# Optimization experiments

Measured on AMD Instinct MI355X. Metric: run time of the kernel, lower is better.

Reference implementation:

```python
import jax, jax.numpy as jnp
import numpy as np

T, D_ENC, H, D_EMB, VOCAB = 4000, 1024, 1024, 512, 8192
V = VOCAB + 1  # + blank
P = 800
TEMPERATURE = 1.0


def setup_inputs() -> dict:
    key = jax.random.key(0)
    ks = jax.random.split(key, 8)
    s = lambda d: 1.0 / np.sqrt(d)
    return {
        'enc_out': jax.random.normal(ks[0], (T, D_ENC), jnp.float32),
        'embedding': jax.random.normal(ks[1], (V, D_EMB), jnp.float32) * s(D_EMB),
        'W_ih': jax.random.normal(ks[2], (4 * H, D_EMB), jnp.float32) * s(D_EMB),
        'W_hh': jax.random.normal(ks[3], (4 * H, H), jnp.float32) * s(H),
        'b_lstm': jnp.zeros((4 * H,), jnp.float32),
        'W_pred': jax.random.normal(ks[4], (D_ENC, H), jnp.float32) * s(H),
        'b_pred': jnp.zeros((D_ENC,), jnp.float32),
        'W_join': jax.random.normal(ks[5], (V, D_ENC), jnp.float32) * s(D_ENC),
        'b_join': jnp.zeros((V,), jnp.float32),
        'phonemes': jax.random.randint(ks[6], (P,), 0, VOCAB, jnp.int32),
    }


def reference(enc_out, embedding, W_ih, W_hh, b_lstm, W_pred, b_pred, W_join, b_join, phonemes):
    blank_idx = embedding.shape[0] - 1
    n_phon = phonemes.shape[0]

    def predict_step(tok, h, c):
        # one-token RNNT predictor: embed -> LSTM cell -> projection to joiner dim
        x = embedding[tok]
        gates = x @ W_ih.T + h @ W_hh.T + b_lstm  # [4H]
        i, f, g, o = jnp.split(gates, 4)
        i, f, o = jax.nn.sigmoid(i), jax.nn.sigmoid(f), jax.nn.sigmoid(o)
        c2 = f * c + i * jnp.tanh(g)
        h2 = o * jnp.tanh(c2)
        pred = h2 @ W_pred.T + b_pred  # [D_ENC]
        return pred, h2, c2

    def step(carry, enc_t):
        tok, h, c, tp = carry
        pred, h2, c2 = predict_step(tok, h, c)
        logits = (jax.nn.relu(enc_t + pred) @ W_join.T + b_join) / TEMPERATURE
        logp = jax.nn.log_softmax(logits)  # [V]
        pick = jnp.argmax(logp)
        phon_done = tp >= n_phon
        is_blank = (pick == blank_idx) | phon_done
        next_phon = phonemes[jnp.minimum(tp, n_phon - 1)]
        prediction = jnp.where(is_blank, blank_idx, next_phon)
        # blank: keep hypothesis token/state; non-blank: advance to phoneme + new state
        tok2 = jnp.where(is_blank, tok, next_phon)
        h3 = jnp.where(is_blank, h, h2)
        c3 = jnp.where(is_blank, c, c2)
        tp2 = tp + jnp.where(is_blank, 0, 1)
        return (tok2, h3, c3, tp2), (logp, prediction, ~phon_done)

    # initial predictor pass with blank token from zero state (mirrors the warm-up predict call)
    h0 = jnp.zeros((W_hh.shape[1],), enc_out.dtype)
    c0 = jnp.zeros_like(h0)
    _, h_init, c_init = predict_step(jnp.int32(blank_idx), h0, c0)
    carry0 = (jnp.int32(blank_idx), h_init, c_init, jnp.int32(0))
    _, (alignment, predictions, valid) = jax.lax.scan(step, carry0, enc_out)
    return alignment, predictions, valid
```

## Files before the change

kernel.cpp:

```cpp
#include <hip/hip_runtime.h>
#include <math.h>

#define TT     4000
#define DENC   1024
#define HD     1024
#define DEMB   512
#define VD     8193
#define NPH    800
#define BLANK  8192
#define NWG    256
#define NTHR   512
#define CHUNK_M 800
#define NSTEP  (NPH + 2)
#define NSTEPP 802
#define NVT    65
#define NP     129
#define CHUNK  256

typedef __bf16 bf16x4 __attribute__((ext_vector_type(4)));
typedef __bf16 bf16x8 __attribute__((ext_vector_type(8)));
typedef float  f32x16 __attribute__((ext_vector_type(16)));

#define MEMSET_BYTES 20480
#define WSF_HX     1024
#define WSF_HHIST  5120
#define WSF_PREDS  826368
#define WSF_GXT    826368
#define WSF_PMAX   1646592
#define WSF_PSUM   2162592
#define WSF_PARG   2678592
#define WSF_LSE    3194592
#define WSF_AMAX   3198592
#define WSF_XBF    3199616
#define WSF_W16    4903552
#define WSF_END    9163392
#define NEED_MFMA  ((size_t)WSF_END * 4)
#define TST_IDX    512
#define F_PMAX 1646592
#define F_PSUM 1906592
#define F_PARG 2166592
#define F_LSE  2426592

#define GEMM_SMEM  12800
#define CHAIN_SMEM ((16 * NSTEPP + 2048 + 64) * 4)
#define JOIN_SMEM  (65536 + 128)
#define S_XH   0
#define S_GS   3072
#define S_C4   3088
#define S_TOK  3264
#define S_RED  4066
#define S_AMAX 4082
#define SMEM_FLOATS_F32 4352
#define SMEM_BYTES_F32 (SMEM_FLOATS_F32 * 4)


__device__ __forceinline__ float dot4(float4 a, float4 b, float acc) {
  acc = fmaf(a.x, b.x, acc); acc = fmaf(a.y, b.y, acc);
  acc = fmaf(a.z, b.z, acc); acc = fmaf(a.w, b.w, acc);
  return acc;
}
__device__ __forceinline__ float sigmf(float x) { return 1.f / (1.f + expf(-x)); }
__device__ __forceinline__ float sigm_fast(float x) { return 1.f / (1.f + __expf(-x)); }
__device__ __forceinline__ float tanh_fast(float x) {
  float e = __expf(2.f * x);
  return 1.f - 2.f / (e + 1.f);
}

__device__ __forceinline__ void combine3(float& m, float& s, int& am,
                                         float om, float os, int oa) {
  float mm = fmaxf(m, om);
  s = s * __expf(m - mm) + os * __expf(om - mm);
  if (om > m || (om == m && oa < am)) am = oa;
  m = mm;
}

__device__ __forceinline__ void gload16(const void* g, void* l) {
  __builtin_amdgcn_global_load_lds(
      (const __attribute__((address_space(1))) unsigned int*)g,
      (__attribute__((address_space(3))) unsigned int*)l, 16, 0, 0);
}

__device__ __forceinline__ float ld_coh(const float* p) {
  return __hip_atomic_load((const float*)p, __ATOMIC_RELAXED, __HIP_MEMORY_SCOPE_AGENT);
}

__device__ __forceinline__ void light_barrier(unsigned* flags, unsigned& ep) {
  unsigned* arrive  = flags;
  unsigned* release = flags + 256;
  __builtin_amdgcn_s_waitcnt(0);
  __syncthreads();
  if (blockIdx.x == 0) {
    int tid = threadIdx.x;
    if (tid > 0 && tid < NWG) {
      while (__hip_atomic_load(&arrive[tid], __ATOMIC_RELAXED, __HIP_MEMORY_SCOPE_AGENT) != ep) {}
    }
    __syncthreads();
    if (tid == 0)
      __hip_atomic_store(release, ep, __ATOMIC_RELAXED, __HIP_MEMORY_SCOPE_AGENT);
  } else {
    if (threadIdx.x == 0) {
      __hip_atomic_store(&arrive[blockIdx.x], ep, __ATOMIC_RELAXED, __HIP_MEMORY_SCOPE_AGENT);
      while (__hip_atomic_load(release, __ATOMIC_RELAXED, __HIP_MEMORY_SCOPE_AGENT) != ep) {}
    }
    __syncthreads();
  }
  asm volatile("" ::: "memory");
  ep++;
}

__device__ __forceinline__ void heavy_barrier(unsigned* flags) {
  unsigned* bar = flags + 257;
  __syncthreads();
  if (threadIdx.x == 0) {
    __threadfence();
    unsigned g = __hip_atomic_load(&bar[1], __ATOMIC_RELAXED, __HIP_MEMORY_SCOPE_AGENT);
    unsigned v = __hip_atomic_fetch_add(&bar[0], 1u, __ATOMIC_RELAXED, __HIP_MEMORY_SCOPE_AGENT);
    if (v == (unsigned)(NWG - 1)) {
      __hip_atomic_store(&bar[0], 0u, __ATOMIC_RELAXED, __HIP_MEMORY_SCOPE_AGENT);
      __hip_atomic_store(&bar[1], g + 1u, __ATOMIC_RELEASE, __HIP_MEMORY_SCOPE_AGENT);
    } else {
      while (__hip_atomic_load(&bar[1], __ATOMIC_RELAXED, __HIP_MEMORY_SCOPE_AGENT) == g)
        __builtin_amdgcn_s_sleep(1);
    }
    __threadfence();
  }
  __syncthreads();
}

__device__ void xbf_fill(const float* enc, const float* preds, __bf16* dst,
                         int t0, int K, int pi0, int g0, int gs) {
  int total = K << 8;
  for (int q = g0; q < total; q += gs) {
    int j = q >> 8, seg = q & 255;
    int pi = (pi0 < 0) ? NPH : pi0 + j;
    float4 e = ((const float4*)(enc + (size_t)(t0 + j) * 1024))[seg];
    float4 p = ((const float4*)(preds + (size_t)pi * 1024))[seg];
    bf16x4 r;
    r[0] = (__bf16)fmaxf(e.x + p.x, 0.f);
    r[1] = (__bf16)fmaxf(e.y + p.y, 0.f);
    r[2] = (__bf16)fmaxf(e.z + p.z, 0.f);
    r[3] = (__bf16)fmaxf(e.w + p.w, 0.f);
    *(bf16x4*)(dst + (size_t)j * 1024 + (seg << 2)) = r;
  }
}

__device__ void joiner_tiles(const __bf16* W16, const __bf16* xrows, const float* bj,
                             float* out_align, float* pmax, float* psum, int* parg,
                             char* smc, int t0, int K, int tile0, int tstride) {
  const int tid = threadIdx.x;
  const int wid = tid >> 6, lane = tid & 63;
  const int wj = wid & 3, wv = wid >> 2;
  const int l31 = lane & 31, lhi = lane >> 5;
  const int jt_n = (K + 127) >> 7;
  const int ntiles = jt_n * NVT;

  for (int tile = tile0; tile < ntiles; tile += tstride) {
    const int vt = tile % NVT, jt = tile / NVT;
    const int v0 = vt << 7, j0 = jt << 7;
    f32x16 acc0, acc1;
    #pragma unroll
    for (int i = 0; i < 16; ++i) { acc0[i] = 0.f; acc1[i] = 0.f; }

    auto stage = [&](int db, int kb) {
      char* wb = smc + db * 32768;
      char* xb = wb + 16384;
      #pragma unroll
      for (int p = 0; p < 2; ++p) {
        int sbase = p * 512 + wid * 64;
        int s = sbase + lane;
        int ks = s >> 7, r = s & 127;
        gload16(W16 + (size_t)(v0 + r) * 1024 + kb + ks * 8, wb + sbase * 16);
        gload16(xrows + (size_t)(j0 + r) * 1024 + kb + ks * 8, xb + sbase * 16);
      }
    };

    stage(0, 0);
    __syncthreads();
    int db = 0;
    for (int kb16 = 0; kb16 < 16; ++kb16) {
      if (kb16 < 15) stage(db ^ 1, (kb16 + 1) << 6);
      const char* wb = smc + db * 32768;
      const char* xb = wb + 16384;
      #pragma unroll
      for (int k16 = 0; k16 < 4; ++k16) {
        int ks = k16 * 2 + lhi;
        bf16x8 a  = *(const bf16x8*)(xb + ((ks << 7) + (wj << 5) + l31) * 16);
        bf16x8 b0 = *(const bf16x8*)(wb + ((ks << 7) + (wv << 6) + l31) * 16);
        bf16x8 b1 = *(const bf16x8*)(wb + ((ks << 7) + (wv << 6) + 32 + l31) * 16);
        acc0 = __builtin_amdgcn_mfma_f32_32x32x16_bf16(a, b0, acc0, 0, 0, 0);
        acc1 = __builtin_amdgcn_mfma_f32_32x32x16_bf16(a, b1, acc1, 0, 0, 0);
      }
      __syncthreads();
      db ^= 1;
    }

    const int v_0 = v0 + (wv << 6) + l31;
    const int v_1 = v_0 + 32;
    const float bj0 = (v_0 < VD) ? bj[v_0] : 0.f;
    const float bj1 = (v_1 < VD) ? bj[v_1] : 0.f;
    const int jbase = j0 + (wj << 5) + 4 * lhi;
    const bool npok = (v0 + (wv << 6)) < VD;
    const int np = (v0 >> 6) + wv;
    #pragma unroll
    for (int reg = 0; reg < 16; ++reg) {
      int j = jbase + (reg & 3) + 8 * (reg >> 2);
      bool jok = j < K;
      float lg0 = acc0[reg] + bj0;
      float lg1 = acc1[reg] + bj1;
      if (jok) {
        size_t ro = (size_t)(t0 + j) * VD;
        if (v_0 < VD) out_align[ro + v_0] = lg0;
        if (v_1 < VD) out_align[ro + v_1] = lg1;
      }
      float l0 = (v_0 < VD) ? lg0 : -1e30f;
      float l1 = (v_1 < VD) ? lg1 : -1e30f;
      float m = fmaxf(l0, l1);
      float ss = 0.f;
      if (v_0 < VD) ss += __expf(l0 - m);
      if (v_1 < VD) ss += __expf(l1 - m);
      int am = (l1 > l0) ? v_1 : v_0;
      #pragma unroll
      for (int msk = 1; msk <= 16; msk <<= 1) {
        float om = __shfl_xor(m, msk, 64);
        float os = __shfl_xor(ss, msk, 64);
        int oa = __shfl_xor(am, msk, 64);
        float mm = fmaxf(m, om);
        ss = ss * __expf(m - mm) + os * __expf(om - mm);
        if (om > m || (om == m && oa < am)) am = oa;
        m = mm;
      }
      if (l31 == 0 && jok && npok) {
        size_t pb = (size_t)(t0 + j) * NP + np;
        __hip_atomic_store(&pmax[pb], m, __ATOMIC_RELAXED, __HIP_MEMORY_SCOPE_AGENT);
        __hip_atomic_store(&psum[pb], ss, __ATOMIC_RELAXED, __HIP_MEMORY_SCOPE_AGENT);
        __hip_atomic_store(&parg[pb], am, __ATOMIC_RELAXED, __HIP_MEMORY_SCOPE_AGENT);
      }
    }
  }
}

__device__ __forceinline__ void merge_row129(const float* pmax, const float* psum,
                                             const int* parg, int row, int lane,
                                             float& m, float& s, int& am) {
  size_t b = (size_t)row * NP;
  m = ld_coh(pmax + b + lane);
  s = ld_coh(psum + b + lane);
  am = __hip_atomic_load(&parg[b + lane], __ATOMIC_RELAXED, __HIP_MEMORY_SCOPE_AGENT);
  {
    int i2 = lane + 64;
    float om = ld_coh(pmax + b + i2);
    float os = ld_coh(psum + b + i2);
    int oa = __hip_atomic_load(&parg[b + i2], __ATOMIC_RELAXED, __HIP_MEMORY_SCOPE_AGENT);
    combine3(m, s, am, om, os, oa);
  }
  if (lane == 0) {
    float om = ld_coh(pmax + b + 128);
    float os = ld_coh(psum + b + 128);
    int oa = __hip_atomic_load(&parg[b + 128], __ATOMIC_RELAXED, __HIP_MEMORY_SCOPE_AGENT);
    combine3(m, s, am, om, os, oa);
  }
  #pragma unroll
  for (int msk = 32; msk; msk >>= 1) {
    float om = __shfl_xor(m, msk, 64);
    float os = __shfl_xor(s, msk, 64);
    int oa = __shfl_xor(am, msk, 64);
    combine3(m, s, am, om, os, oa);
  }
}

__global__ __launch_bounds__(512) void wconv_kernel(const float* __restrict__ Wjoin,
                                                    float* wsf) {
  __bf16* w16 = (__bf16*)(wsf + WSF_W16);
  int g0 = blockIdx.x * 512 + threadIdx.x;
  int gs = gridDim.x * 512;
  for (int q = g0; q < VD * 256; q += gs) {
    int v = q >> 8, seg = q & 255;
    float4 w4 = ((const float4*)(Wjoin + (size_t)v * 1024))[seg];
    bf16x4 r;
    r[0] = (__bf16)w4.x; r[1] = (__bf16)w4.y; r[2] = (__bf16)w4.z; r[3] = (__bf16)w4.w;
    *(bf16x4*)(w16 + (size_t)v * 1024 + (seg << 2)) = r;
  }
}

__global__ __launch_bounds__(512) void gx_kernel(
    const float* __restrict__ Wih, const float* __restrict__ emb,
    const float* __restrict__ bl, const int* __restrict__ phon, float* wsf) {
  extern __shared__ float sm[];
  float* Wt = sm;
  float* Xt = sm + 2112;
  float* gxT = wsf + WSF_GXT;
  const int tid = threadIdx.x;
  const int tx = tid & 31, ty = tid >> 5;
  int ntiles = 32 * 13;
  for (int tile = blockIdx.x; tile < ntiles; tile += gridDim.x) {
    int vt = tile & 31, jt = tile >> 5;
    int v0 = vt * 128, j0 = jt * 64;
    float acc[4][4];
    #pragma unroll
    for (int a = 0; a < 4; ++a)
      #pragma unroll
      for (int q = 0; q < 4; ++q) acc[a][q] = 0.f;
    for (int kk = 0; kk < DEMB; kk += 16) {
      {
        int r = tid >> 2, seg = tid & 3;
        float4 wv = ((const float4*)(Wih + (size_t)(v0 + r) * DEMB + kk))[seg];
        Wt[(seg * 4 + 0) * 132 + r] = wv.x;
        Wt[(seg * 4 + 1) * 132 + r] = wv.y;
        Wt[(seg * 4 + 2) * 132 + r] = wv.z;
        Wt[(seg * 4 + 3) * 132 + r] = wv.w;
      }
      if (tid < 256) {
        int r = tid >> 2, seg = tid & 3;
        int j = j0 + r;
        float4 xv = make_float4(0.f, 0.f, 0.f, 0.f);
        if (j < NSTEP) {
          int tok = (j < 2) ? BLANK : phon[j - 2];
          xv = ((const float4*)(emb + (size_t)tok * DEMB + kk))[seg];
        }
        Xt[(seg * 4 + 0) * 68 + r] = xv.x;
        Xt[(seg * 4 + 1) * 68 + r] = xv.y;
        Xt[(seg * 4 + 2) * 68 + r] = xv.z;
        Xt[(seg * 4 + 3) * 68 + r] = xv.w;
      }
      __syncthreads();
      #pragma unroll
      for (int k = 0; k < 16; ++k) {
        float4 a = *(const float4*)(Wt + k * 132 + (tx << 2));
        float4 bq = *(const float4*)(Xt + k * 68 + (ty << 2));
        acc[0][0] = fmaf(a.x, bq.x, acc[0][0]); acc[1][0] = fmaf(a.y, bq.x, acc[1][0]);
        acc[2][0] = fmaf(a.z, bq.x, acc[2][0]); acc[3][0] = fmaf(a.w, bq.x, acc[3][0]);
        acc[0][1] = fmaf(a.x, bq.y, acc[0][1]); acc[1][1] = fmaf(a.y, bq.y, acc[1][1]);
        acc[2][1] = fmaf(a.z, bq.y, acc[2][1]); acc[3][1] = fmaf(a.w, bq.y, acc[3][1]);
        acc[0][2] = fmaf(a.x, bq.z, acc[0][2]); acc[1][2] = fmaf(a.y, bq.z, acc[1][2]);
        acc[2][2] = fmaf(a.z, bq.z, acc[2][2]); acc[3][2] = fmaf(a.w, bq.z, acc[3][2]);
        acc[0][3] = fmaf(a.x, bq.w, acc[0][3]); acc[1][3] = fmaf(a.y, bq.w, acc[1][3]);
        acc[2][3] = fmaf(a.z, bq.w, acc[2][3]); acc[3][3] = fmaf(a.w, bq.w, acc[3][3]);
      }
      __syncthreads();
    }
    int vb = v0 + (tx << 2), jb0 = j0 + (ty << 2);
    #pragma unroll
    for (int jj = 0; jj < 4; ++jj) {
      int j = jb0 + jj;
      if (j >= NSTEP) continue;
      #pragma unroll
      for (int q = 0; q < 4; ++q)
        gxT[(size_t)(vb + q) * NSTEPP + j] = acc[q][jj] + bl[vb + q];
    }
  }
}

__global__ __launch_bounds__(NTHR) void chain_kernel(const float* __restrict__ Whh,
                                                     float* wsf) {
  extern __shared__ float sm[];
  float* gxl = sm;
  float* hb  = sm + 16 * NSTEPP;
  float* GS  = hb + 2048;
  const int tid = threadIdx.x;
  const int w = tid >> 6, l = tid & 63;
  const int b = blockIdx.x;
  const float* gxT = wsf + WSF_GXT;
  float* hhist = wsf + WSF_HHIST;
  unsigned long long* hx = (unsigned long long*)(wsf + WSF_HX);

  float4 W0[4], W1[4];
  {
    int rr0 = 2 * w, rr1 = 2 * w + 1;
    int gr0 = ((rr0 >> 2) << 10) + 4 * b + (rr0 & 3);
    int gr1 = ((rr1 >> 2) << 10) + 4 * b + (rr1 & 3);
    const float4* h0 = (const float4*)(Whh + (size_t)gr0 * HD);
    const float4* h1 = (const float4*)(Whh + (size_t)gr1 * HD);
    #pragma unroll
    for (int i = 0; i < 4; ++i) { W0[i] = h0[l + 64 * i]; W1[i] = h1[l + 64 * i]; }
  }
  for (int rr = 0; rr < 16; ++rr) {
    int gr = ((rr >> 2) << 10) + 4 * b + (rr & 3);
    for (int s = tid; s < NSTEP; s += NTHR)
      gxl[rr * NSTEPP + s] = gxT[(size_t)gr * NSTEPP + s];
  }
  for (int i = tid; i < 1024; i += NTHR) hb[i] = 0.f;
  __syncthreads();

  float c_reg = 0.f;
  for (int s = 0; s < NSTEP; ++s) {
    int p = s & 1;
    const float4* h4 = (const float4*)(hb + p * 1024);
    float a0 = 0.f, a1 = 0.f;
    #pragma unroll
    for (int i = 0; i < 4; ++i) {
      float4 hv = h4[l + 64 * i];
      a0 = dot4(W0[i], hv, a0);
      a1 = dot4(W1[i], hv, a1);
    }
    #pragma unroll
    for (int m = 32; m; m >>= 1) {
      a0 += __shfl_xor(a0, m, 64);
      a1 += __shfl_xor(a1, m, 64);
    }
    if (l == 0) { GS[2 * w] = a0; GS[2 * w + 1] = a1; }
    __syncthreads();
    if (tid < 4) {
      int j = tid;
      float gi = GS[j]      + gxl[j * NSTEPP + s];
      float gf = GS[4 + j]  + gxl[(4 + j) * NSTEPP + s];
      float gg = GS[8 + j]  + gxl[(8 + j) * NSTEPP + s];
      float go = GS[12 + j] + gxl[(12 + j) * NSTEPP + s];
      float c2 = sigm_fast(gf) * c_reg + sigm_fast(gi) * tanh_fast(gg);
      float h2 = sigm_fast(go) * tanh_fast(c2);
      c_reg = c2;
      int cell = 4 * b + j;
      hhist[(size_t)s * HD + cell] = h2;
      unsigned long long pk = ((unsigned long long)(unsigned)(s + 1) << 32)
                            | (unsigned long long)__float_as_uint(h2);
      __hip_atomic_store(&hx[(p ^ 1) * 1024 + cell], pk,
                         __ATOMIC_RELAXED, __HIP_MEMORY_SCOPE_AGENT);
    }
    if (s + 1 < NSTEP) {
      unsigned tg = (unsigned)(s + 1);
      const unsigned long long* src = hx + (p ^ 1) * 1024;
      unsigned long long v0, v1;
      do {
        v0 = __hip_atomic_load(&src[2 * tid],     __ATOMIC_RELAXED, __HIP_MEMORY_SCOPE_AGENT);
        v1 = __hip_atomic_load(&src[2 * tid + 1], __ATOMIC_RELAXED, __HIP_MEMORY_SCOPE_AGENT);
      } while ((unsigned)(v0 >> 32) != tg || (unsigned)(v1 >> 32) != tg);
      float* dst = hb + (p ^ 1) * 1024 + 2 * tid;
      dst[0] = __uint_as_float((unsigned)v0);
      dst[1] = __uint_as_float((unsigned)v1);
    }
    __syncthreads();
  }
}

__global__ __launch_bounds__(512) void preds_kernel(
    const float* __restrict__ Wpred, const float* __restrict__ bp, float* wsf) {
  extern __shared__ float sm[];
  float* Wt = sm;
  float* Xt = sm + 2112;
  const float* hhist = wsf + WSF_HHIST;
  float* preds = wsf + WSF_PREDS;
  const int tid = threadIdx.x;
  const int tx = tid & 31, ty = tid >> 5;
  int ntiles = 8 * 13;
  for (int tile = blockIdx.x; tile < ntiles; tile += gridDim.x) {
    int vt = tile & 7, jt = tile >> 3;
    int v0 = vt * 128, j0 = jt * 64;
    float acc[4][4];
    #pragma unroll
    for (int a = 0; a < 4; ++a)
      #pragma unroll
      for (int q = 0; q < 4; ++q) acc[a][q] = 0.f;
    for (int kk = 0; kk < 1024; kk += 16) {
      {
        int r = tid >> 2, seg = tid & 3;
        float4 wv = ((const float4*)(Wpred + (size_t)(v0 + r) * HD + kk))[seg];
        Wt[(seg * 4 + 0) * 132 + r] = wv.x;
        Wt[(seg * 4 + 1) * 132 + r] = wv.y;
        Wt[(seg * 4 + 2) * 132 + r] = wv.z;
        Wt[(seg * 4 + 3) * 132 + r] = wv.w;
      }
      if (tid < 256) {
        int r = tid >> 2, seg = tid & 3;
        int j = j0 + r;
        float4 xv = make_float4(0.f, 0.f, 0.f, 0.f);
        if (j <= NPH) xv = ((const float4*)(hhist + (size_t)(j + 1) * HD + kk))[seg];
        Xt[(seg * 4 + 0) * 68 + r] = xv.x;
        Xt[(seg * 4 + 1) * 68 + r] = xv.y;
        Xt[(seg * 4 + 2) * 68 + r] = xv.z;
        Xt[(seg * 4 + 3) * 68 + r] = xv.w;
      }
      __syncthreads();
      #pragma unroll
      for (int k = 0; k < 16; ++k) {
        float4 a = *(const float4*)(Wt + k * 132 + (tx << 2));
        float4 bq = *(const float4*)(Xt + k * 68 + (ty << 2));
        acc[0][0] = fmaf(a.x, bq.x, acc[0][0]); acc[1][0] = fmaf(a.y, bq.x, acc[1][0]);
        acc[2][0] = fmaf(a.z, bq.x, acc[2][0]); acc[3][0] = fmaf(a.w, bq.x, acc[3][0]);
        acc[0][1] = fmaf(a.x, bq.y, acc[0][1]); acc[1][1] = fmaf(a.y, bq.y, acc[1][1]);
        acc[2][1] = fmaf(a.z, bq.y, acc[2][1]); acc[3][1] = fmaf(a.w, bq.y, acc[3][1]);
        acc[0][2] = fmaf(a.x, bq.z, acc[0][2]); acc[1][2] = fmaf(a.y, bq.z, acc[1][2]);
        acc[2][2] = fmaf(a.z, bq.z, acc[2][2]); acc[3][2] = fmaf(a.w, bq.z, acc[3][2]);
        acc[0][3] = fmaf(a.x, bq.w, acc[0][3]); acc[1][3] = fmaf(a.y, bq.w, acc[1][3]);
        acc[2][3] = fmaf(a.z, bq.w, acc[2][3]); acc[3][3] = fmaf(a.w, bq.w, acc[3][3]);
      }
      __syncthreads();
    }
    int vb = v0 + (tx << 2), jb0 = j0 + (ty << 2);
    #pragma unroll
    for (int jj = 0; jj < 4; ++jj) {
      int j = jb0 + jj;
      if (j > NPH) continue;
      #pragma unroll
      for (int q = 0; q < 4; ++q)
        preds[(size_t)j * 1024 + vb + q] = acc[q][jj] + bp[vb + q];
    }
  }
}

__global__ void xspec_kernel(const float* __restrict__ enc, float* wsf) {
  xbf_fill(enc, wsf + WSF_PREDS, (__bf16*)(wsf + WSF_XBF), 0, CHUNK_M, 0,
           blockIdx.x * blockDim.x + threadIdx.x, gridDim.x * blockDim.x);
}

__global__ __launch_bounds__(NTHR) void joinspec_kernel(const float* __restrict__ bj,
                                                        float* out, float* wsf) {
  extern __shared__ float sm[];
  joiner_tiles((__bf16*)(wsf + WSF_W16), (__bf16*)(wsf + WSF_XBF), bj, out,
               wsf + WSF_PMAX, wsf + WSF_PSUM, (int*)(wsf + WSF_PARG),
               (char*)sm, 0, CHUNK_M, blockIdx.x, gridDim.x);
}

__global__ __launch_bounds__(NTHR) void decode_coop(
    const float* enc, const float* bj, const int* phon, float* out, float* wsf) {
  extern __shared__ float sm[];
  char* smc = (char*)sm;
  unsigned* flags = (unsigned*)wsf;
  float* preds = wsf + WSF_PREDS;
  float* pmax = wsf + WSF_PMAX;
  float* psum = wsf + WSF_PSUM;
  int* parg = (int*)(wsf + WSF_PARG);
  float* lse = wsf + WSF_LSE;
  int* amaxws = (int*)(wsf + WSF_AMAX);
  __bf16* xbf = (__bf16*)(wsf + WSF_XBF);
  __bf16* w16 = (__bf16*)(wsf + WSF_W16);
  float* out_pred  = out + (size_t)TT * VD;
  float* out_valid = out + (size_t)TT * VD + TT;

  const int tid = threadIdx.x;
  const int wid = tid >> 6, lane = tid & 63;
  unsigned ep = 1;
  int t = 0, tp = 0, iter = 0;

  while (t < TT && tp < NPH) {
    int K = CHUNK_M;
    if (TT - t < K) K = TT - t;
    if (NPH - tp < K) K = NPH - tp;
    if (iter > 0) {
      heavy_barrier(flags);
      xbf_fill(enc, preds, xbf, t, K, tp, blockIdx.x * NTHR + tid, gridDim.x * NTHR);
      heavy_barrier(flags);
      joiner_tiles(w16, xbf, bj, out, pmax, psum, parg, smc, t, K,
                   blockIdx.x, gridDim.x);
    }
    light_barrier(flags, ep);
    for (int j = blockIdx.x * 8 + wid; j < K; j += gridDim.x * 8) {
      float m, s; int am;
      merge_row129(pmax, psum, parg, t + j, lane, m, s, am);
      if (lane == 0) {
        __hip_atomic_store(&amaxws[j], am, __ATOMIC_RELAXED, __HIP_MEMORY_SCOPE_AGENT);
        lse[t + j] = m + logf(s);
      }
    }
    light_barrier(flags, ep);
    int cand = K;
    for (int idx = tid; idx < K; idx += NTHR) {
      int a = __hip_atomic_load(&amaxws[idx], __ATOMIC_RELAXED, __HIP_MEMORY_SCOPE_AGENT);
      if (a == BLANK && idx < cand) cand = idx;
    }
    #pragma unroll
    for (int msk = 32; msk; msk >>= 1) cand = min(cand, __shfl_xor(cand, msk, 64));
    int* red = (int*)(smc + 65536);
    if (lane == 0) red[wid] = cand;
    __syncthreads();
    if (tid == 0) {
      int mn = red[0];
      for (int w2 = 1; w2 < 8; ++w2) mn = min(mn, red[w2]);
      red[8] = mn;
    }
    __syncthreads();
    int jb = red[8];
    __syncthreads();
    int nacc = (jb < K) ? jb + 1 : K;
    int nadv = (jb < K) ? jb : K;
    if (blockIdx.x == 0) {
      for (int j = tid; j < nacc; j += NTHR) {
        out_pred[t + j] = (j == jb) ? (float)BLANK : (float)phon[tp + j];
        out_valid[t + j] = 1.f;
      }
    }
    t += nacc; tp += nadv; ++iter;
  }

  if (t < TT) {
    xbf_fill(enc, preds, xbf + (size_t)(t - 800) * 1024, t, TT - t, -1,
             blockIdx.x * NTHR + tid, gridDim.x * NTHR);
  }
  if (blockIdx.x == 0 && tid == 0) ((int*)wsf)[TST_IDX] = t;
}

__global__ __launch_bounds__(NTHR) void jointail_kernel(const float* __restrict__ bj,
                                                        float* out, float* wsf) {
  extern __shared__ float sm[];
  int t = ((const int*)wsf)[TST_IDX];
  if (t >= TT) return;
  joiner_tiles((__bf16*)(wsf + WSF_W16),
               (__bf16*)(wsf + WSF_XBF) + (size_t)(t - 800) * 1024, bj, out,
               wsf + WSF_PMAX, wsf + WSF_PSUM, (int*)(wsf + WSF_PARG),
               (char*)sm, t, TT - t, blockIdx.x, gridDim.x);
}

__global__ __launch_bounds__(NTHR) void mergetail_kernel(float* out, float* wsf) {
  int t = ((const int*)wsf)[TST_IDX];
  float* lse = wsf + WSF_LSE;
  float* out_pred  = out + (size_t)TT * VD;
  float* out_valid = out + (size_t)TT * VD + TT;
  const int wid = threadIdx.x >> 6, lane = threadIdx.x & 63;
  for (int row = t + blockIdx.x * 8 + wid; row < TT; row += gridDim.x * 8) {
    float m, s; int am;
    merge_row129(wsf + WSF_PMAX, wsf + WSF_PSUM, (const int*)(wsf + WSF_PARG),
                 row, lane, m, s, am);
    if (lane == 0) {
      lse[row] = m + logf(s);
      out_pred[row] = (float)BLANK;
      out_valid[row] = 0.f;
    }
  }
}

__global__ __launch_bounds__(256) void sub_kernel(float* out, const float* wsf) {
  const float* lse = wsf + WSF_LSE;
  for (int row = blockIdx.x; row < TT; row += gridDim.x) {
    float l = lse[row];
    float* p = out + (size_t)row * VD;
    for (int i = threadIdx.x; i < VD; i += 256) p[i] -= l;
  }
}

struct Ctx {
  const float *enc, *emb, *Wih, *Whh, *bl, *Wpred, *bp, *Wjoin, *bj;
  const int* phon;
  unsigned long long* hx;
  float *hhist, *preds, *pmax, *psum, *lse;
  int* parg;
  unsigned* flags;
  float *out_align, *out_pred, *out_valid;
};

__device__ void chain_all_legacy(const Ctx& C, float* sm) {
  const int tid = threadIdx.x;
  const int w = tid >> 6, l = tid & 63;
  const int b = blockIdx.x;
  int* tok_sm = (int*)(sm + S_TOK);
  for (int s = tid; s < NSTEP; s += NTHR)
    tok_sm[s] = (s < 2) ? BLANK : C.phon[s - 2];
  float4 W0[6], W1[6];
  {
    int rr0 = 2 * w, rr1 = 2 * w + 1;
    int gr0 = ((rr0 >> 2) << 10) + 4 * b + (rr0 & 3);
    int gr1 = ((rr1 >> 2) << 10) + 4 * b + (rr1 & 3);
    const float4* ih0 = (const float4*)(C.Wih + (size_t)gr0 * DEMB);
    const float4* hh0 = (const float4*)(C.Whh + (size_t)gr0 * HD);
    const float4* ih1 = (const float4*)(C.Wih + (size_t)gr1 * DEMB);
    const float4* hh1 = (const float4*)(C.Whh + (size_t)gr1 * HD);
    W0[0] = ih0[l];       W0[1] = ih0[64 + l];
    W0[2] = hh0[l];       W0[3] = hh0[64 + l];
    W0[4] = hh0[128 + l]; W0[5] = hh0[192 + l];
    W1[0] = ih1[l];       W1[1] = ih1[64 + l];
    W1[2] = hh1[l];       W1[3] = hh1[64 + l];
    W1[4] = hh1[128 + l]; W1[5] = hh1[192 + l];
  }
  float bi = 0.f, bf = 0.f, bg = 0.f, bo = 0.f;
  if (tid < 4) {
    bi = C.bl[4 * b + tid];
    bf = C.bl[1024 + 4 * b + tid];
    bg = C.bl[2048 + 4 * b + tid];
    bo = C.bl[3072 + 4 * b + tid];
    sm[S_C4 + tid] = 0.f;
  }
  for (int i = tid; i < 1536; i += NTHR) sm[S_XH + i] = 0.f;
  if (tid < 512) sm[S_XH + tid] = C.emb[(size_t)BLANK * DEMB + tid];
  __syncthreads();
  unsigned long long* hx = C.hx;
  for (int s = 0; s < NSTEP; ++s) {
    int p = s & 1;
    const float4* xh4 = (const float4*)(sm + S_XH + p * 1536);
    float a0 = 0.f, a1 = 0.f;
    #pragma unroll
    for (int i = 0; i < 6; ++i) {
      float4 v = xh4[i * 64 + l];
      a0 = dot4(W0[i], v, a0);
      a1 = dot4(W1[i], v, a1);
    }
    #pragma unroll
    for (int m = 32; m; m >>= 1) {
      a0 += __shfl_xor(a0, m, 64);
      a1 += __shfl_xor(a1, m, 64);
    }
    if (l == 0) { sm[S_GS + 2 * w] = a0; sm[S_GS + 2 * w + 1] = a1; }
    if (s + 1 < NSTEP && tid < 512)
      sm[S_XH + (1 - p) * 1536 + tid] = C.emb[(size_t)tok_sm[s + 1] * DEMB + tid];
    __syncthreads();
    if (tid < 4) {
      int j = tid;
      float gi = sm[S_GS + j]      + bi;
      float gf = sm[S_GS + 4 + j]  + bf;
      float gg = sm[S_GS + 8 + j]  + bg;
      float go = sm[S_GS + 12 + j] + bo;
      float cc = sm[S_C4 + j];
      float c2 = sigmf(gf) * cc + sigmf(gi) * tanhf(gg);
      float h2 = sigmf(go) * tanhf(c2);
      sm[S_C4 + j] = c2;
      int cell = 4 * b + j;
      C.hhist[(size_t)s * HD + cell] = h2;
      unsigned long long pk = ((unsigned long long)(unsigned)(s + 1) << 32)
                            | (unsigned long long)__float_as_uint(h2);
      __hip_atomic_store(&hx[(1 - p) * 1024 + cell], pk,
                         __ATOMIC_RELAXED, __HIP_MEMORY_SCOPE_AGENT);
    }
    if (s + 1 < NSTEP) {
      unsigned tg = (unsigned)(s + 1);
      #pragma unroll
      for (int kq = 0; kq < 2; ++kq) {
        int k = tid + kq * 512;
        unsigned long long v;
        do {
          v = __hip_atomic_load(&hx[(1 - p) * 1024 + k],
                                __ATOMIC_RELAXED, __HIP_MEMORY_SCOPE_AGENT);
        } while ((unsigned)(v >> 32) != tg);
        sm[S_XH + (1 - p) * 1536 + 512 + k] = __uint_as_float((unsigned)v);
      }
    }
    __syncthreads();
  }
}

__device__ void preds_gemm_legacy(const Ctx& C, float* sm) {
  float* Wt = sm;
  float* Xt = sm + 2112;
  const int tid = threadIdx.x;
  const int tx = tid & 31, ty = tid >> 5;
  int ntiles = 8 * 13;
  for (int tile = blockIdx.x; tile < ntiles; tile += NWG) {
    int vt = tile & 7, jt = tile >> 3;
    int v0 = vt * 128, j0 = jt * 64;
    float acc[4][4];
    #pragma unroll
    for (int a = 0; a < 4; ++a)
      #pragma unroll
      for (int q = 0; q < 4; ++q) acc[a][q] = 0.f;
    for (int kk = 0; kk < 1024; kk += 16) {
      {
        int r = tid >> 2, seg = tid & 3;
        float4 wv = ((const float4*)(C.Wpred + (size_t)(v0 + r) * HD + kk))[seg];
        Wt[(seg * 4 + 0) * 132 + r] = wv.x;
        Wt[(seg * 4 + 1) * 132 + r] = wv.y;
        Wt[(seg * 4 + 2) * 132 + r] = wv.z;
        Wt[(seg * 4 + 3) * 132 + r] = wv.w;
      }
      if (tid < 256) {
        int r = tid >> 2, seg = tid & 3;
        int j = j0 + r;
        float4 xv = make_float4(0.f, 0.f, 0.f, 0.f);
        if (j <= NPH) xv = ((const float4*)(C.hhist + (size_t)(j + 1) * HD + kk))[seg];
        Xt[(seg * 4 + 0) * 68 + r] = xv.x;
        Xt[(seg * 4 + 1) * 68 + r] = xv.y;
        Xt[(seg * 4 + 2) * 68 + r] = xv.z;
        Xt[(seg * 4 + 3) * 68 + r] = xv.w;
      }
      __syncthreads();
      #pragma unroll
      for (int k = 0; k < 16; ++k) {
        float4 a = *(const float4*)(Wt + k * 132 + (tx << 2));
        float4 bq = *(const float4*)(Xt + k * 68 + (ty << 2));
        acc[0][0] = fmaf(a.x, bq.x, acc[0][0]); acc[1][0] = fmaf(a.y, bq.x, acc[1][0]);
        acc[2][0] = fmaf(a.z, bq.x, acc[2][0]); acc[3][0] = fmaf(a.w, bq.x, acc[3][0]);
        acc[0][1] = fmaf(a.x, bq.y, acc[0][1]); acc[1][1] = fmaf(a.y, bq.y, acc[1][1]);
        acc[2][1] = fmaf(a.z, bq.y, acc[2][1]); acc[3][1] = fmaf(a.w, bq.y, acc[3][1]);
        acc[0][2] = fmaf(a.x, bq.z, acc[0][2]); acc[1][2] = fmaf(a.y, bq.z, acc[1][2]);
        acc[2][2] = fmaf(a.z, bq.z, acc[2][2]); acc[3][2] = fmaf(a.w, bq.z, acc[3][2]);
        acc[0][3] = fmaf(a.x, bq.w, acc[0][3]); acc[1][3] = fmaf(a.y, bq.w, acc[1][3]);
        acc[2][3] = fmaf(a.z, bq.w, acc[2][3]); acc[3][3] = fmaf(a.w, bq.w, acc[3][3]);
      }
      __syncthreads();
    }
    int vb = v0 + (tx << 2), jb0 = j0 + (ty << 2);
    #pragma unroll
    for (int jj = 0; jj < 4; ++jj) {
      int j = jb0 + jj;
      if (j > NPH) continue;
      #pragma unroll
      for (int q = 0; q < 4; ++q)
        C.preds[(size_t)j * 1024 + vb + q] = acc[q][jj] + C.bp[vb + q];
    }
  }
}

__device__ void joiner_gemm_f32(const Ctx& C, float* sm, int t0, int K, int pi0) {
  float* Wt = sm;
  float* Xt = sm + 2112;
  const int tid = threadIdx.x;
  const int tx = tid & 31, ty = tid >> 5;
  int jt_n = (K + 63) >> 6;
  int ntiles = jt_n * NVT;
  for (int tile = blockIdx.x; tile < ntiles; tile += NWG) {
    int vt = tile % NVT, jt = tile / NVT;
    int v0 = vt * 128, j0 = jt * 64;
    float acc[4][4];
    #pragma unroll
    for (int a = 0; a < 4; ++a)
      #pragma unroll
      for (int q = 0; q < 4; ++q) acc[a][q] = 0.f;
    for (int kk = 0; kk < 1024; kk += 16) {
      {
        int r = tid >> 2, seg = tid & 3;
        int v = v0 + r;
        float4 wv = make_float4(0.f, 0.f, 0.f, 0.f);
        if (v < VD) wv = ((const float4*)(C.Wjoin + (size_t)v * 1024 + kk))[seg];
        Wt[(seg * 4 + 0) * 132 + r] = wv.x;
        Wt[(seg * 4 + 1) * 132 + r] = wv.y;
        Wt[(seg * 4 + 2) * 132 + r] = wv.z;
        Wt[(seg * 4 + 3) * 132 + r] = wv.w;
      }
      if (tid < 256) {
        int r = tid >> 2, seg = tid & 3;
        int j = j0 + r;
        float4 xv = make_float4(0.f, 0.f, 0.f, 0.f);
        if (j < K) {
          int pi = (pi0 < 0) ? NPH : (pi0 + j);
          float4 e = ((const float4*)(C.enc + (size_t)(t0 + j) * DENC + kk))[seg];
          float4 pr = ((const float4*)(C.preds + (size_t)pi * 1024 + kk))[seg];
          xv.x = fmaxf(e.x + pr.x, 0.f);
          xv.y = fmaxf(e.y + pr.y, 0.f);
          xv.z = fmaxf(e.z + pr.z, 0.f);
          xv.w = fmaxf(e.w + pr.w, 0.f);
        }
        Xt[(seg * 4 + 0) * 68 + r] = xv.x;
        Xt[(seg * 4 + 1) * 68 + r] = xv.y;
        Xt[(seg * 4 + 2) * 68 + r] = xv.z;
        Xt[(seg * 4 + 3) * 68 + r] = xv.w;
      }
      __syncthreads();
      #pragma unroll
      for (int k = 0; k < 16; ++k) {
        float4 a = *(const float4*)(Wt + k * 132 + (tx << 2));
        float4 bq = *(const float4*)(Xt + k * 68 + (ty << 2));
        acc[0][0] = fmaf(a.x, bq.x, acc[0][0]); acc[1][0] = fmaf(a.y, bq.x, acc[1][0]);
        acc[2][0] = fmaf(a.z, bq.x, acc[2][0]); acc[3][0] = fmaf(a.w, bq.x, acc[3][0]);
        acc[0][1] = fmaf(a.x, bq.y, acc[0][1]); acc[1][1] = fmaf(a.y, bq.y, acc[1][1]);
        acc[2][1] = fmaf(a.z, bq.y, acc[2][1]); acc[3][1] = fmaf(a.w, bq.y, acc[3][1]);
        acc[0][2] = fmaf(a.x, bq.z, acc[0][2]); acc[1][2] = fmaf(a.y, bq.z, acc[1][2]);
        acc[2][2] = fmaf(a.z, bq.z, acc[2][2]); acc[3][2] = fmaf(a.w, bq.z, acc[3][2]);
        acc[0][3] = fmaf(a.x, bq.w, acc[0][3]); acc[1][3] = fmaf(a.y, bq.w, acc[1][3]);
        acc[2][3] = fmaf(a.z, bq.w, acc[2][3]); acc[3][3] = fmaf(a.w, bq.w, acc[3][3]);
      }
      __syncthreads();
    }
    int vb = v0 + (tx << 2);
    int jb0 = j0 + (ty << 2);
    float bjv[4];
    #pragma unroll
    for (int q = 0; q < 4; ++q) bjv[q] = (vb + q < VD) ? C.bj[vb + q] : 0.f;
    #pragma unroll
    for (int jj = 0; jj < 4; ++jj) {
      int j = jb0 + jj;
      if (j >= K) continue;
      size_t ro = (size_t)(t0 + j) * VD;
      float lg[4];
      float m = -1e30f; int am = vb;
      #pragma unroll
      for (int q = 0; q < 4; ++q) {
        int v = vb + q;
        if (v < VD) {
          lg[q] = acc[q][jj] + bjv[q];
          C.out_align[ro + v] = lg[q];
          if (lg[q] > m) { m = lg[q]; am = v; }
        } else lg[q] = -1e30f;
      }
      float ss = 0.f;
      #pragma unroll
      for (int q = 0; q < 4; ++q)
        if (vb + q < VD) ss += __expf(lg[q] - m);
      #pragma unroll
      for (int msk = 16; msk; msk >>= 1) {
        float om = __shfl_xor(m, msk, 64);
        float os = __shfl_xor(ss, msk, 64);
        int oa = __shfl_xor(am, msk, 64);
        combine3(m, ss, am, om, os, oa);
      }
      if (tx == 0) {
        size_t pb = (size_t)(t0 + j) * NVT + vt;
        __hip_atomic_store(&C.pmax[pb], m, __ATOMIC_RELAXED, __HIP_MEMORY_SCOPE_AGENT);
        __hip_atomic_store(&C.psum[pb], ss, __ATOMIC_RELAXED, __HIP_MEMORY_SCOPE_AGENT);
        __hip_atomic_store(&C.parg[pb], am, __ATOMIC_RELAXED, __HIP_MEMORY_SCOPE_AGENT);
      }
    }
  }
}

__device__ __forceinline__ void merge_row65(const Ctx& C, int row, int lane,
                                            float& m, float& s, int& am) {
  size_t b = (size_t)row * NVT;
  m = ld_coh(C.pmax + b + lane);
  s = ld_coh(C.psum + b + lane);
  am = __hip_atomic_load(&C.parg[b + lane], __ATOMIC_RELAXED, __HIP_MEMORY_SCOPE_AGENT);
  if (lane == 0) {
    float om = ld_coh(C.pmax + b + 64);
    float os = ld_coh(C.psum + b + 64);
    int oa = __hip_atomic_load(&C.parg[b + 64], __ATOMIC_RELAXED, __HIP_MEMORY_SCOPE_AGENT);
    combine3(m, s, am, om, os, oa);
  }
  #pragma unroll
  for (int msk = 32; msk; msk >>= 1) {
    float om = __shfl_xor(m, msk, 64);
    float os = __shfl_xor(s, msk, 64);
    int oa = __shfl_xor(am, msk, 64);
    combine3(m, s, am, om, os, oa);
  }
}

__global__ __launch_bounds__(NTHR) void decode_kernel_f32(
    const float* enc, const float* emb, const float* Wih, const float* Whh,
    const float* bl, const float* Wpred, const float* bp, const float* Wjoin,
    const float* bj, const int* phon, float* out, float* wsf) {
  extern __shared__ float sm[];
  Ctx C;
  C.enc = enc; C.emb = emb; C.Wih = Wih; C.Whh = Whh; C.bl = bl;
  C.Wpred = Wpred; C.bp = bp; C.Wjoin = Wjoin; C.bj = bj; C.phon = phon;
  C.flags = (unsigned*)wsf;
  C.hx = (unsigned long long*)(wsf + WSF_HX);
  C.hhist = wsf + WSF_HHIST;
  C.preds = wsf + WSF_PREDS;
  C.pmax = wsf + F_PMAX;
  C.psum = wsf + F_PSUM;
  C.parg = (int*)(wsf + F_PARG);
  C.lse = wsf + F_LSE;
  C.out_align = out;
  C.out_pred  = out + (size_t)TT * VD;
  C.out_valid = out + (size_t)TT * VD + TT;

  const int tid = threadIdx.x;
  const int wid = tid >> 6, lane = tid & 63;
  unsigned ep = 1;

  chain_all_legacy(C, sm);
  heavy_barrier(C.flags);
  preds_gemm_legacy(C, sm);
  heavy_barrier(C.flags);

  int t = 0, tp = 0;
  while (t < TT && tp < NPH) {
    int K = CHUNK;
    if (TT - t < K) K = TT - t;
    if (NPH - tp < K) K = NPH - tp;
    joiner_gemm_f32(C, sm, t, K, tp);
    light_barrier(C.flags, ep);
    int* amax_l = (int*)(sm + S_AMAX);
    for (int j = wid; j < K; j += 8) {
      float m, s; int am;
      merge_row65(C, t + j, lane, m, s, am);
      if (lane == 0) {
        amax_l[j] = am;
        C.lse[t + j] = m + logf(s);
      }
    }
    __syncthreads();
    int cand = K;
    if (tid < K && amax_l[tid] == BLANK) cand = tid;
    #pragma unroll
    for (int msk = 32; msk; msk >>= 1) cand = min(cand, __shfl_xor(cand, msk, 64));
    int* red = (int*)(sm + S_RED);
    if (lane == 0) red[wid] = cand;
    __syncthreads();
    if (tid == 0) {
      int mn = red[0];
      for (int w2 = 1; w2 < 8; ++w2) mn = min(mn, red[w2]);
      red[8] = mn;
    }
    __syncthreads();
    int jb = red[8];
    __syncthreads();
    int nacc = (jb < K) ? jb + 1 : K;
    int nadv = (jb < K) ? jb : K;
    if (blockIdx.x == 0) {
      int* tok_sm = (int*)(sm + S_TOK);
      for (int j = tid; j < nacc; j += NTHR) {
        C.out_pred[t + j] = (j == jb) ? (float)BLANK : (float)tok_sm[tp + j + 2];
        C.out_valid[t + j] = 1.f;
      }
    }
    t += nacc; tp += nadv;
    if (jb < K) heavy_barrier(C.flags);
  }
  if (t < TT) {
    int Kt = TT - t;
    joiner_gemm_f32(C, sm, t, Kt, -1);
    light_barrier(C.flags, ep);
    for (int i = blockIdx.x * 8 + wid; i < Kt; i += NWG * 8) {
      float m, s; int am;
      merge_row65(C, t + i, lane, m, s, am);
      if (lane == 0) C.lse[t + i] = m + logf(s);
    }
    const int gtid = blockIdx.x * NTHR + tid;
    for (int i = gtid; i < Kt; i += NWG * NTHR) {
      C.out_pred[t + i] = (float)BLANK;
      C.out_valid[t + i] = 0.f;
    }
  }
  heavy_barrier(C.flags);
  for (int row = blockIdx.x; row < TT; row += NWG) {
    float l = C.lse[row];
    float* p = C.out_align + (size_t)row * VD;
    for (int i = tid; i < VD; i += NTHR) p[i] -= l;
  }
}


extern "C" void kernel_launch(void* const* d_in, const int* in_sizes, int n_in,
                              void* d_out, int out_size, void* d_ws, size_t ws_size,
                              hipStream_t stream) {
  const float* enc   = (const float*)d_in[0];
  const float* emb   = (const float*)d_in[1];
  const float* Wih   = (const float*)d_in[2];
  const float* Whh   = (const float*)d_in[3];
  const float* bl    = (const float*)d_in[4];
  const float* Wpred = (const float*)d_in[5];
  const float* bp    = (const float*)d_in[6];
  const float* Wjoin = (const float*)d_in[7];
  const float* bj    = (const float*)d_in[8];
  const int*   phon  = (const int*)d_in[9];
  float* out = (float*)d_out;
  float* wsf = (float*)d_ws;

  hipMemsetAsync(d_ws, 0, MEMSET_BYTES, stream);

  if (ws_size >= NEED_MFMA) {
    hipFuncSetAttribute((const void*)chain_kernel,
                        hipFuncAttributeMaxDynamicSharedMemorySize, CHAIN_SMEM);
    hipFuncSetAttribute((const void*)joinspec_kernel,
                        hipFuncAttributeMaxDynamicSharedMemorySize, JOIN_SMEM);
    hipFuncSetAttribute((const void*)decode_coop,
                        hipFuncAttributeMaxDynamicSharedMemorySize, JOIN_SMEM);
    hipFuncSetAttribute((const void*)jointail_kernel,
                        hipFuncAttributeMaxDynamicSharedMemorySize, JOIN_SMEM);

    wconv_kernel<<<1024, 512, 0, stream>>>(Wjoin, wsf);
    gx_kernel<<<416, 512, GEMM_SMEM, stream>>>(Wih, emb, bl, phon, wsf);
    {
      const float* WhhA = Whh; float* wsfA = wsf;
      void* a2[] = { &WhhA, &wsfA };
      hipError_t e = hipLaunchCooperativeKernel((void*)chain_kernel, dim3(256), dim3(NTHR),
                                                a2, CHAIN_SMEM, stream);
      if (e != hipSuccess)
        chain_kernel<<<dim3(256), dim3(NTHR), CHAIN_SMEM, stream>>>(Whh, wsf);
    }
    preds_kernel<<<104, 512, GEMM_SMEM, stream>>>(Wpred, bp, wsf);
    xspec_kernel<<<1024, 256, 0, stream>>>(enc, wsf);
    joinspec_kernel<<<455, NTHR, JOIN_SMEM, stream>>>(bj, out, wsf);
    {
      const float* encA = enc; const float* bjA = bj; const int* phonA = phon;
      float* outA = out; float* wsfA = wsf;
      void* a3[] = { &encA, &bjA, &phonA, &outA, &wsfA };
      hipError_t e = hipLaunchCooperativeKernel((void*)decode_coop, dim3(NWG), dim3(NTHR),
                                                a3, JOIN_SMEM, stream);
      if (e != hipSuccess)
        decode_coop<<<dim3(NWG), dim3(NTHR), JOIN_SMEM, stream>>>(enc, bj, phon, out, wsf);
    }
    jointail_kernel<<<1664, NTHR, JOIN_SMEM, stream>>>(bj, out, wsf);
    mergetail_kernel<<<256, NTHR, 0, stream>>>(out, wsf);
    sub_kernel<<<2048, 256, 0, stream>>>(out, wsf);
  } else {
    hipFuncSetAttribute((const void*)decode_kernel_f32,
                        hipFuncAttributeMaxDynamicSharedMemorySize, SMEM_BYTES_F32);
    void* args[] = { &enc, &emb, &Wih, &Whh, &bl, &Wpred, &bp, &Wjoin, &bj, &phon, &out, &wsf };
    hipError_t e = hipLaunchCooperativeKernel((void*)decode_kernel_f32, dim3(NWG), dim3(NTHR),
                                              args, SMEM_BYTES_F32, stream);
    if (e != hipSuccess) {
      decode_kernel_f32<<<dim3(NWG), dim3(NTHR), SMEM_BYTES_F32, stream>>>(
          enc, emb, Wih, Whh, bl, Wpred, bp, Wjoin, bj, phon, out, wsf);
    }
  }
}
```

Before: 2.705 ms.

## Exchange LSTM hidden state as packed bf16 slots with sentinel polling

The recurrent chain kernel now publishes each block's four hidden values as one packed 64-bit bf16 word in a per-step slot, pre-filled with a 0xFF sentinel. Readers poll only their own slot with s_sleep backoff instead of checking 1024 fp32 entries tagged with a step number. This reduces the cross-block traffic and the polling cost per recurrent step. The gate pre-activations gx are also stored in bf16 to halve their size and shared memory use. In exchange the recurrent hidden state and the input gates are rounded to bf16, which can affect accuracy and argmax decisions, and an extra memset of the slot array is added.

```diff
diff --git a/kernel.cpp b/kernel.cpp
--- a/kernel.cpp
+++ b/kernel.cpp
@@ -21,28 +21,33 @@
 typedef __bf16 bf16x8 __attribute__((ext_vector_type(8)));
 typedef float  f32x16 __attribute__((ext_vector_type(16)));
 
-#define MEMSET_BYTES 20480
-#define WSF_HX     1024
-#define WSF_HHIST  5120
-#define WSF_PREDS  826368
-#define WSF_GXT    826368
-#define WSF_PMAX   1646592
-#define WSF_PSUM   2162592
-#define WSF_PARG   2678592
-#define WSF_LSE    3194592
-#define WSF_AMAX   3198592
-#define WSF_XBF    3199616
-#define WSF_W16    4903552
-#define WSF_END    9163392
-#define NEED_MFMA  ((size_t)WSF_END * 4)
+#define WSF_HHIST  1024
+#define WSF_PREDS  822272
+#define WSF_HX     1642496
+#define WSF_GXT    2053120
+#define WSF_PMAX   1642496
+#define WSF_PSUM   2158496
+#define WSF_PARG   2674496
+#define WSF_LSE    3190496
+#define WSF_AMAX   3194496
+#define WSF_XBF    3195520
+#define WSF_W16    4899456
+#define WSF_END    9159296
+#define NEED_MFMA  ((size_t)36653568)
 #define TST_IDX    512
+#define HX_BYTE_OFF  ((size_t)WSF_HX * 4)
+#define HX_BYTES     ((size_t)NSTEPP * 256 * 8)
+
+#define L_HX     1024
+#define L_HHIST  5120
+#define L_PREDS  826368
 #define F_PMAX 1646592
 #define F_PSUM 1906592
 #define F_PARG 2166592
 #define F_LSE  2426592
 
 #define GEMM_SMEM  12800
-#define CHAIN_SMEM ((16 * NSTEPP + 2048 + 64) * 4)
+#define CHAIN_SMEM (4096 + 64 + 16 * NSTEPP * 2)
 #define JOIN_SMEM  (65536 + 128)
 #define S_XH   0
 #define S_GS   3072
@@ -64,6 +69,9 @@
 __device__ __forceinline__ float tanh_fast(float x) {
   float e = __expf(2.f * x);
   return 1.f - 2.f / (e + 1.f);
+}
+__device__ __forceinline__ float bfbits_to_f32(unsigned u16v) {
+  return __builtin_bit_cast(float, (u16v & 0xFFFFu) << 16);
 }
 
 __device__ __forceinline__ void combine3(float& m, float& s, int& am,
@@ -288,7 +296,7 @@
   extern __shared__ float sm[];
   float* Wt = sm;
   float* Xt = sm + 2112;
-  float* gxT = wsf + WSF_GXT;
+  __bf16* gxT = (__bf16*)(wsf + WSF_GXT);
   const int tid = threadIdx.x;
   const int tx = tid & 31, ty = tid >> 5;
   int ntiles = 32 * 13;
@@ -345,7 +353,7 @@
       if (j >= NSTEP) continue;
       #pragma unroll
       for (int q = 0; q < 4; ++q)
-        gxT[(size_t)(vb + q) * NSTEPP + j] = acc[q][jj] + bl[vb + q];
+        gxT[(size_t)(vb + q) * NSTEPP + j] = (__bf16)(acc[q][jj] + bl[vb + q]);
     }
   }
 }
@@ -353,13 +361,13 @@
 __global__ __launch_bounds__(NTHR) void chain_kernel(const float* __restrict__ Whh,
                                                      float* wsf) {
   extern __shared__ float sm[];
-  float* gxl = sm;
-  float* hb  = sm + 16 * NSTEPP;
-  float* GS  = hb + 2048;
+  float* hcur = sm;
+  float* GS = sm + 1024;
+  __bf16* gxl = (__bf16*)(sm + 1024 + 16);
   const int tid = threadIdx.x;
   const int w = tid >> 6, l = tid & 63;
   const int b = blockIdx.x;
-  const float* gxT = wsf + WSF_GXT;
+  const __bf16* gxT = (const __bf16*)(wsf + WSF_GXT);
   float* hhist = wsf + WSF_HHIST;
   unsigned long long* hx = (unsigned long long*)(wsf + WSF_HX);
 
@@ -378,13 +386,12 @@
     for (int s = tid; s < NSTEP; s += NTHR)
       gxl[rr * NSTEPP + s] = gxT[(size_t)gr * NSTEPP + s];
   }
-  for (int i = tid; i < 1024; i += NTHR) hb[i] = 0.f;
+  for (int i = tid; i < 1024; i += NTHR) hcur[i] = 0.f;
   __syncthreads();
 
   float c_reg = 0.f;
   for (int s = 0; s < NSTEP; ++s) {
-    int p = s & 1;
-    const float4* h4 = (const float4*)(hb + p * 1024);
+    const float4* h4 = (const float4*)hcur;
     float a0 = 0.f, a1 = 0.f;
     #pragma unroll
     for (int i = 0; i < 4; ++i) {
@@ -399,33 +406,52 @@
     }
     if (l == 0) { GS[2 * w] = a0; GS[2 * w + 1] = a1; }
     __syncthreads();
+
+    unsigned hb16 = 0;
     if (tid < 4) {
       int j = tid;
-      float gi = GS[j]      + gxl[j * NSTEPP + s];
-      float gf = GS[4 + j]  + gxl[(4 + j) * NSTEPP + s];
-      float gg = GS[8 + j]  + gxl[(8 + j) * NSTEPP + s];
-      float go = GS[12 + j] + gxl[(12 + j) * NSTEPP + s];
+      float gi = GS[j]      + (float)gxl[j * NSTEPP + s];
+      float gf = GS[4 + j]  + (float)gxl[(4 + j) * NSTEPP + s];
+      float gg = GS[8 + j]  + (float)gxl[(8 + j) * NSTEPP + s];
+      float go = GS[12 + j] + (float)gxl[(12 + j) * NSTEPP + s];
       float c2 = sigm_fast(gf) * c_reg + sigm_fast(gi) * tanh_fast(gg);
       float h2 = sigm_fast(go) * tanh_fast(c2);
       c_reg = c2;
-      int cell = 4 * b + j;
-      hhist[(size_t)s * HD + cell] = h2;
-      unsigned long long pk = ((unsigned long long)(unsigned)(s + 1) << 32)
-                            | (unsigned long long)__float_as_uint(h2);
-      __hip_atomic_store(&hx[(p ^ 1) * 1024 + cell], pk,
-                         __ATOMIC_RELAXED, __HIP_MEMORY_SCOPE_AGENT);
-    }
-    if (s + 1 < NSTEP) {
-      unsigned tg = (unsigned)(s + 1);
-      const unsigned long long* src = hx + (p ^ 1) * 1024;
-      unsigned long long v0, v1;
-      do {
-        v0 = __hip_atomic_load(&src[2 * tid],     __ATOMIC_RELAXED, __HIP_MEMORY_SCOPE_AGENT);
-        v1 = __hip_atomic_load(&src[2 * tid + 1], __ATOMIC_RELAXED, __HIP_MEMORY_SCOPE_AGENT);
-      } while ((unsigned)(v0 >> 32) != tg || (unsigned)(v1 >> 32) != tg);
-      float* dst = hb + (p ^ 1) * 1024 + 2 * tid;
-      dst[0] = __uint_as_float((unsigned)v0);
-      dst[1] = __uint_as_float((unsigned)v1);
+      hhist[(size_t)s * HD + 4 * b + j] = h2;
+      __bf16 hb = (__bf16)h2;
+      hb16 = (unsigned)__builtin_bit_cast(unsigned short, hb);
+    }
+    if (w == 0) {
+      unsigned b0 = __shfl(hb16, 0, 64), b1 = __shfl(hb16, 1, 64);
+      unsigned b2 = __shfl(hb16, 2, 64), b3 = __shfl(hb16, 3, 64);
+      if (l == 0) {
+        if (s + 1 < NSTEP) {
+          unsigned long long pk = (unsigned long long)b0
+                                | ((unsigned long long)b1 << 16)
+                                | ((unsigned long long)b2 << 32)
+                                | ((unsigned long long)b3 << 48);
+          __hip_atomic_store(&hx[(size_t)s * 256 + b], pk,
+                             __ATOMIC_RELAXED, __HIP_MEMORY_SCOPE_AGENT);
+        }
+        float4 hf;
+        hf.x = bfbits_to_f32(b0); hf.y = bfbits_to_f32(b1);
+        hf.z = bfbits_to_f32(b2); hf.w = bfbits_to_f32(b3);
+        ((float4*)hcur)[b] = hf;
+      }
+    }
+    if (s + 1 < NSTEP && tid < 256 && tid != b) {
+      const unsigned long long* src = &hx[(size_t)s * 256 + tid];
+      unsigned long long v = __hip_atomic_load(src, __ATOMIC_RELAXED, __HIP_MEMORY_SCOPE_AGENT);
+      while ((v & 0xFFFFull) == 0xFFFFull) {
+        __builtin_amdgcn_s_sleep(1);
+        v = __hip_atomic_load(src, __ATOMIC_RELAXED, __HIP_MEMORY_SCOPE_AGENT);
+      }
+      float4 hf;
+      hf.x = bfbits_to_f32((unsigned)v);
+      hf.y = bfbits_to_f32((unsigned)(v >> 16));
+      hf.z = bfbits_to_f32((unsigned)(v >> 32));
+      hf.w = bfbits_to_f32((unsigned)(v >> 48));
+      ((float4*)hcur)[tid] = hf;
     }
     __syncthreads();
   }
@@ -916,9 +942,9 @@
   C.enc = enc; C.emb = emb; C.Wih = Wih; C.Whh = Whh; C.bl = bl;
   C.Wpred = Wpred; C.bp = bp; C.Wjoin = Wjoin; C.bj = bj; C.phon = phon;
   C.flags = (unsigned*)wsf;
-  C.hx = (unsigned long long*)(wsf + WSF_HX);
-  C.hhist = wsf + WSF_HHIST;
-  C.preds = wsf + WSF_PREDS;
+  C.hx = (unsigned long long*)(wsf + L_HX);
+  C.hhist = wsf + L_HHIST;
+  C.preds = wsf + L_PREDS;
   C.pmax = wsf + F_PMAX;
   C.psum = wsf + F_PSUM;
   C.parg = (int*)(wsf + F_PARG);
@@ -1020,9 +1046,11 @@
   float* out = (float*)d_out;
   float* wsf = (float*)d_ws;
 
-  hipMemsetAsync(d_ws, 0, MEMSET_BYTES, stream);
+  hipMemsetAsync(d_ws, 0, 20480, stream);
 
   if (ws_size >= NEED_MFMA) {
+    hipMemsetAsync((char*)d_ws + HX_BYTE_OFF, 0xFF, HX_BYTES, stream);
+
     hipFuncSetAttribute((const void*)chain_kernel,
                         hipFuncAttributeMaxDynamicSharedMemorySize, CHAIN_SMEM);
     hipFuncSetAttribute((const void*)joinspec_kernel,
```

Measured after the change: 3.284 ms. +21.4%, slower.
